# Performance work log

Hardware: AMD Instinct MI355X
Metric: run time of the kernel (lower is better)

Reference implementation:

```python
import jax, jax.numpy as jnp
import numpy as np

B, T, D, H = 4, 2048, 1024, 16
DK = D // H

def setup_inputs() -> dict:
    key = jax.random.key(0)
    ks = jax.random.split(key, 10)
    s = 1.0 / np.sqrt(D)
    inp = {
        'x': jax.random.normal(ks[0], (B, T, D), dtype=jnp.float32),
        'mask': jnp.tril(jnp.ones((T, T), dtype=jnp.int32))[None, None, :, :],
        'Wq': jax.random.normal(ks[1], (D, D), dtype=jnp.float32) * s,
        'bq': jnp.zeros((D,), dtype=jnp.float32),
        'Wk': jax.random.normal(ks[2], (D, D), dtype=jnp.float32) * s,
        'bk': jnp.zeros((D,), dtype=jnp.float32),
        'Wv': jax.random.normal(ks[3], (D, D), dtype=jnp.float32) * s,
        'bv': jnp.zeros((D,), dtype=jnp.float32),
        'Wo': jax.random.normal(ks[4], (D, D), dtype=jnp.float32) * s,
        'bo': jnp.zeros((D,), dtype=jnp.float32),
    }
    return inp

def reference(x, mask, Wq, bq, Wk, bk, Wv, bv, Wo, bo):
    # Project and split heads: [B,T,D] -> [B,H,T,DK]
    def heads(w, b):
        return (x @ w.T + b).reshape(B, T, H, DK).transpose(0, 2, 1, 3)
    q, k, v = heads(Wq, bq), heads(Wk, bk), heads(Wv, bv)
    scores = jnp.einsum('bhqd,bhkd->bhqk', q, k) / np.sqrt(DK).astype(jnp.float32)
    scores = jnp.where(mask[:, :, :T, :T] == 0, jnp.float32(-1e10), scores)
    prob = jax.nn.softmax(scores, axis=-1)
    y = jnp.einsum('bhqk,bhkd->bhqd', prob, v)  # [B,H,T,DK]
    y = y.transpose(0, 2, 1, 3).reshape(B, T, D)
    return y @ Wo.T + bo
```

## Files before the change

### kernel.cpp

```cpp
#include <hip/hip_runtime.h>


typedef unsigned short u16;
typedef unsigned int   u32;
using bf16x8 = __attribute__((ext_vector_type(8))) short;
using f32x4  = __attribute__((ext_vector_type(4))) float;
using u32x4  = __attribute__((ext_vector_type(4))) u32;

#define DEVINL __device__ __forceinline__
#define AS1 __attribute__((address_space(1)))
#define AS3 __attribute__((address_space(3)))

DEVINL u16 f2bf(float f) {
  u32 u = __builtin_bit_cast(u32, f);
  u32 r = u + 0x7fffu + ((u >> 16) & 1u);
  return (u16)(r >> 16);
}
DEVINL u32 pk2(float a, float b) {
  u32 ua = __builtin_bit_cast(u32, a) + 0x8000u;
  u32 ub = __builtin_bit_cast(u32, b) + 0x8000u;
  return (ua >> 16) | (ub & 0xffff0000u);
}
DEVINL float exp2fast(float x) {
#if __has_builtin(__builtin_amdgcn_exp2f)
  return __builtin_amdgcn_exp2f(x);
#else
  return __builtin_exp2f(x);
#endif
}
DEVINL void gload16(const u16* g, u16* l) {
  __builtin_amdgcn_global_load_lds((const AS1 u32*)g, (AS3 u32*)l, 16, 0, 0);
}

__global__ __launch_bounds__(256) void cvt_f32_bf16(const float* __restrict__ in,
                                                    u16* __restrict__ out, int n4) {
  int i = blockIdx.x * 256 + threadIdx.x;
  if (i < n4) {
    float4 v = reinterpret_cast<const float4*>(in)[i];
    u32 lo = (u32)f2bf(v.x) | ((u32)f2bf(v.y) << 16);
    u32 hi = (u32)f2bf(v.z) | ((u32)f2bf(v.w) << 16);
    reinterpret_cast<uint2*>(out)[i] = make_uint2(lo, hi);
  }
}

DEVINL void gemm_core(const u16* __restrict__ Ag, const u16* __restrict__ Bg,
                      int m0, int n0, f32x4 acc[4][4], u16* Al, u16* Bl, int tid) {
  const int lane = tid & 63, wave = tid >> 6;
  const int wr = wave >> 1, wc = wave & 1;
  const int lr = lane & 15, lg = lane >> 4;
  const int srow = wave * 32 + (lane >> 2);
  const int scol = ((lane & 3) * 8) ^ ((srow & 3) << 3);
  for (int kt = 0; kt < 1024; kt += 32) {
    __syncthreads();
    const u16* ga = Ag + (size_t)(m0 + srow) * 1024 + kt + scol;
    gload16(ga,             Al + wave * 1024);
    gload16(ga + 16 * 1024, Al + wave * 1024 + 512);
    const u16* gb = Bg + (size_t)(n0 + srow) * 1024 + kt + scol;
    gload16(gb,             Bl + wave * 1024);
    gload16(gb + 16 * 1024, Bl + wave * 1024 + 512);
    __syncthreads();
    bf16x8 af[4], bfr[4];
#pragma unroll
    for (int t = 0; t < 4; t++) {
      int ra = wr * 64 + t * 16 + lr;
      af[t] = *reinterpret_cast<const bf16x8*>(
          reinterpret_cast<const char*>(Al) + ra * 64 + ((lg * 16) ^ ((ra & 3) << 4)));
      int rb = wc * 64 + t * 16 + lr;
      bfr[t] = *reinterpret_cast<const bf16x8*>(
          reinterpret_cast<const char*>(Bl) + rb * 64 + ((lg * 16) ^ ((rb & 3) << 4)));
    }
#pragma unroll
    for (int mi = 0; mi < 4; mi++)
#pragma unroll
      for (int ni = 0; ni < 4; ni++)
        acc[mi][ni] = __builtin_amdgcn_mfma_f32_16x16x32_bf16(af[mi], bfr[ni], acc[mi][ni], 0, 0, 0);
  }
}

__global__ __launch_bounds__(256) void qkv_gemm(
    const u16* __restrict__ xb,
    const u16* __restrict__ wqb, const u16* __restrict__ wkb, const u16* __restrict__ wvb,
    const float* __restrict__ bq, const float* __restrict__ bk, const float* __restrict__ bv,
    u16* __restrict__ qb, u16* __restrict__ kb, u16* __restrict__ vb) {
  __shared__ __align__(16) u16 smem[8192];
  u16* Al = smem;
  u16* Bl = smem + 4096;
  const int z = blockIdx.z;
  const u16* W = (z == 0) ? wqb : (z == 1) ? wkb : wvb;
  const float* bias = (z == 0) ? bq : (z == 1) ? bk : bv;
  const int m0 = blockIdx.x * 128, n0 = blockIdx.y * 128;
  f32x4 acc[4][4];
#pragma unroll
  for (int a = 0; a < 4; a++)
#pragma unroll
    for (int b2 = 0; b2 < 4; b2++) acc[a][b2] = f32x4{0.f, 0.f, 0.f, 0.f};
  gemm_core(xb, W, m0, n0, acc, Al, Bl, threadIdx.x);
  const int lane = threadIdx.x & 63, wave = threadIdx.x >> 6;
  const int wr = wave >> 1, wc = wave & 1, lr = lane & 15, lg = lane >> 4;

  if (z == 2) {
    const int b = m0 >> 11, tb = m0 & 2047;
#pragma unroll
    for (int h2 = 0; h2 < 2; ++h2) {
      __syncthreads();
      if (wc == h2) {
#pragma unroll
        for (int mi = 0; mi < 4; mi++)
#pragma unroll
          for (int ni = 0; ni < 4; ni++)
#pragma unroll
            for (int i = 0; i < 4; i++) {
              int t_l = wr * 64 + mi * 16 + lg * 4 + i;
              int dk_l = ni * 16 + lr;
              float v = acc[mi][ni][i] + bias[n0 + h2 * 64 + dk_l];
              int m = t_l & 63;
              int col = (t_l & 64) | (m & 0x23) | ((m & 0x0C) << 1) | ((m & 0x10) >> 2);
              *(u16*)((char*)smem + dk_l * 256 + ((col * 2) ^ ((dk_l & 7) << 4))) = f2bf(v);
            }
      }
      __syncthreads();
      const int hh = (n0 >> 6) + h2;
      u16* vrow = vb + (size_t)(b * 16 + hh) * 64 * 2048 + tb;
#pragma unroll
      for (int i2 = 0; i2 < 4; i2++) {
        int c = (int)threadIdx.x + i2 * 256;
        int dk_l = c >> 4, tc2 = c & 15;
        int4 val = *(const int4*)((const char*)smem + dk_l * 256 + ((tc2 * 16) ^ ((dk_l & 7) << 4)));
        *(int4*)(vrow + (size_t)dk_l * 2048 + tc2 * 8) = val;
      }
    }
    return;
  }

  u16* dst = (z == 0) ? qb : kb;
  const float scl = (z == 0) ? 0.180336880f : 1.0f;
#pragma unroll
  for (int mi = 0; mi < 4; mi++)
#pragma unroll
    for (int ni = 0; ni < 4; ni++)
#pragma unroll
      for (int i = 0; i < 4; i++) {
        int gm = m0 + wr * 64 + mi * 16 + lg * 4 + i;
        int gn = n0 + wc * 64 + ni * 16 + lr;
        float v = (acc[mi][ni][i] + bias[gn]) * scl;
        int b = gm >> 11, t = gm & 2047;
        int h = gn >> 6, dk = gn & 63;
        dst[((size_t)(b * 16 + h) * 2048 + t) * 64 + dk] = f2bf(v);
      }
}

__global__ __launch_bounds__(256) void out_gemm(
    const u16* __restrict__ yb, const u16* __restrict__ wob,
    const float* __restrict__ bo, float* __restrict__ out) {
  __shared__ __align__(16) u16 smem[8192];
  u16* Al = smem;
  u16* Bl = smem + 4096;
  const int m0 = blockIdx.x * 128, n0 = blockIdx.y * 128;
  f32x4 acc[4][4];
#pragma unroll
  for (int a = 0; a < 4; a++)
#pragma unroll
    for (int b2 = 0; b2 < 4; b2++) acc[a][b2] = f32x4{0.f, 0.f, 0.f, 0.f};
  gemm_core(yb, wob, m0, n0, acc, Al, Bl, threadIdx.x);
  const int lane = threadIdx.x & 63, wave = threadIdx.x >> 6;
  const int wr = wave >> 1, wc = wave & 1, lr = lane & 15, lg = lane >> 4;
#pragma unroll
  for (int mi = 0; mi < 4; mi++)
#pragma unroll
    for (int ni = 0; ni < 4; ni++)
#pragma unroll
      for (int i = 0; i < 4; i++) {
        int gm = m0 + wr * 64 + mi * 16 + lg * 4 + i;
        int gn = n0 + wc * 64 + ni * 16 + lr;
        out[(size_t)gm * 1024 + gn] = acc[mi][ni][i] + bo[gn];
      }
}

__global__ __launch_bounds__(256) void attn_fwd(const u16* __restrict__ q_ws,
                                                const u16* __restrict__ k_ws,
                                                const u16* __restrict__ vt_ws,
                                                u16* __restrict__ y_ws) {
  __shared__ __align__(16) u16 Kl[2][4096];
  __shared__ __align__(16) u16 Vt[2][4096];

  const int tid = threadIdx.x;
  const int wave = tid >> 6, lane = tid & 63;
  const int lr = lane & 15, lg = lane >> 4;
  const int qtile = 31 - blockIdx.x;
  const int bh = blockIdx.y;
  const int q0 = qtile * 64;
  const size_t base = (size_t)bh * 2048 * 64;
  const int rgq = q0 + wave * 16 + lr;

  const int srow = wave * 16 + (lane >> 3);
  const int kcol = ((lane & 7) * 8) ^ ((srow & 7) << 3);

  bf16x8 qf[2];
#pragma unroll
  for (int s = 0; s < 2; s++)
    qf[s] = *reinterpret_cast<const bf16x8*>(q_ws + base + (size_t)rgq * 64 + s * 32 + lg * 8);
  asm volatile("s_waitcnt vmcnt(0)" ::: "memory");

  float m_run = -3.0e38f, l_run = 0.f;
  f32x4 oacc[4];
#pragma unroll
  for (int nt = 0; nt < 4; nt++) oacc[nt] = f32x4{0.f, 0.f, 0.f, 0.f};

  auto stage = [&](int buf, int kv0) {
    const u16* kg = k_ws + base + (size_t)(kv0 + srow) * 64 + kcol;
    gload16(kg,           &Kl[buf][wave * 1024]);
    gload16(kg + 8 * 64,  &Kl[buf][wave * 1024 + 512]);
    const u16* vg = vt_ws + base + (size_t)srow * 2048 + kv0 + kcol;
    gload16(vg,            &Vt[buf][wave * 1024]);
    gload16(vg + 8 * 2048, &Vt[buf][wave * 1024 + 512]);
  };

  stage(0, 0);
  int cur = 0;
  for (int t2 = 0; t2 <= qtile; ++t2) {
    const int kv0 = t2 * 64;
    if (t2 < qtile) {
      stage(cur ^ 1, kv0 + 64);
      asm volatile("s_waitcnt vmcnt(4)" ::: "memory");
    } else {
      asm volatile("s_waitcnt vmcnt(0)" ::: "memory");
    }
    __builtin_amdgcn_s_barrier();
    const u16* Kb = Kl[cur];
    const u16* Vb = Vt[cur];

    float sv[4][4];
    __builtin_amdgcn_s_setprio(1);
#pragma unroll
    for (int ct = 0; ct < 4; ct++) {
      f32x4 s = f32x4{0.f, 0.f, 0.f, 0.f};
      int krow = ct * 16 + lr;
#pragma unroll
      for (int s2 = 0; s2 < 2; s2++) {
        bf16x8 kf = *reinterpret_cast<const bf16x8*>(
            reinterpret_cast<const char*>(Kb) + krow * 128 + ((s2 * 64 + lg * 16) ^ ((krow & 7) << 4)));
        s = __builtin_amdgcn_mfma_f32_16x16x32_bf16(kf, qf[s2], s, 0, 0, 0);
      }
#pragma unroll
      for (int i = 0; i < 4; i++) sv[ct][i] = s[i];
    }
    __builtin_amdgcn_s_setprio(0);

    if (t2 == qtile) {
#pragma unroll
      for (int ct = 0; ct < 4; ct++)
#pragma unroll
        for (int i = 0; i < 4; i++)
          if (kv0 + ct * 16 + lg * 4 + i > rgq) sv[ct][i] = -1e30f;
    }

    float cm[4];
#pragma unroll
    for (int ct = 0; ct < 4; ct++)
      cm[ct] = fmaxf(fmaxf(sv[ct][0], sv[ct][1]), fmaxf(sv[ct][2], sv[ct][3]));
    float mx = fmaxf(fmaxf(cm[0], cm[1]), fmaxf(cm[2], cm[3]));
    mx = fmaxf(mx, __shfl_xor(mx, 16, 64));
    mx = fmaxf(mx, __shfl_xor(mx, 32, 64));

    float mnew, alpha;
    const bool nodefer = !__all(mx <= m_run + 8.0f);
    if (nodefer) { mnew = fmaxf(m_run, mx); alpha = exp2fast(m_run - mnew); }
    else         { mnew = m_run;            alpha = 1.0f; }

    float p[4][4];
#pragma unroll
    for (int ct = 0; ct < 4; ct++)
#pragma unroll
      for (int i = 0; i < 4; i++) p[ct][i] = exp2fast(sv[ct][i] - mnew);
    float cs[4];
#pragma unroll
    for (int ct = 0; ct < 4; ct++)
      cs[ct] = (p[ct][0] + p[ct][1]) + (p[ct][2] + p[ct][3]);
    float ps = (cs[0] + cs[1]) + (cs[2] + cs[3]);
    ps += __shfl_xor(ps, 16, 64);
    ps += __shfl_xor(ps, 32, 64);
    l_run = l_run * alpha + ps;
    m_run = mnew;

    u32x4 pw[2];
#pragma unroll
    for (int ks = 0; ks < 2; ks++) {
      pw[ks][0] = pk2(p[2 * ks][0],     p[2 * ks][1]);
      pw[ks][1] = pk2(p[2 * ks][2],     p[2 * ks][3]);
      pw[ks][2] = pk2(p[2 * ks + 1][0], p[2 * ks + 1][1]);
      pw[ks][3] = pk2(p[2 * ks + 1][2], p[2 * ks + 1][3]);
    }

    if (nodefer) {
#pragma unroll
      for (int nt = 0; nt < 4; nt++)
#pragma unroll
        for (int i = 0; i < 4; i++) oacc[nt][i] *= alpha;
    }

    __builtin_amdgcn_s_setprio(1);
#pragma unroll
    for (int nt = 0; nt < 4; nt++) {
      int d = nt * 16 + lr;
#pragma unroll
      for (int ks = 0; ks < 2; ks++) {
        bf16x8 vf = *reinterpret_cast<const bf16x8*>(
            reinterpret_cast<const char*>(Vb) + d * 128 + ((ks * 64 + lg * 16) ^ ((d & 7) << 4)));
        oacc[nt] = __builtin_amdgcn_mfma_f32_16x16x32_bf16(
            vf, __builtin_bit_cast(bf16x8, pw[ks]), oacc[nt], 0, 0, 0);
      }
    }
    __builtin_amdgcn_s_setprio(0);
    __builtin_amdgcn_s_barrier();
    cur ^= 1;
  }

  const float inv = 1.0f / l_run;
  const int b = bh >> 4, h = bh & 15;
#pragma unroll
  for (int nt = 0; nt < 4; nt++) {
    u32 w0 = (u32)f2bf(oacc[nt][0] * inv) | ((u32)f2bf(oacc[nt][1] * inv) << 16);
    u32 w1 = (u32)f2bf(oacc[nt][2] * inv) | ((u32)f2bf(oacc[nt][3] * inv) << 16);
    *reinterpret_cast<uint2*>(y_ws + ((size_t)(b * 2048 + rgq)) * 1024 + h * 64 + nt * 16 + lg * 4) =
        make_uint2(w0, w1);
  }
}

extern "C" void kernel_launch(void* const* d_in, const int* in_sizes, int n_in,
                              void* d_out, int out_size, void* d_ws, size_t ws_size,
                              hipStream_t stream) {
  const float* x  = (const float*)d_in[0];
  const float* Wq = (const float*)d_in[2];
  const float* bq = (const float*)d_in[3];
  const float* Wk = (const float*)d_in[4];
  const float* bk = (const float*)d_in[5];
  const float* Wv = (const float*)d_in[6];
  const float* bv = (const float*)d_in[7];
  const float* Wo = (const float*)d_in[8];
  const float* bo = (const float*)d_in[9];
  float* out = (float*)d_out;

  u16* xb  = (u16*)d_ws;
  u16* wqb = xb  + 8388608;
  u16* wkb = wqb + 1048576;
  u16* wvb = wkb + 1048576;
  u16* wob = wvb + 1048576;
  u16* qb  = wob + 1048576;
  u16* kb  = qb  + 8388608;
  u16* vtb = kb  + 8388608;
  u16* yb  = vtb + 8388608;

  cvt_f32_bf16<<<8192, 256, 0, stream>>>(x,  xb,  2097152);
  cvt_f32_bf16<<<1024, 256, 0, stream>>>(Wq, wqb, 262144);
  cvt_f32_bf16<<<1024, 256, 0, stream>>>(Wk, wkb, 262144);
  cvt_f32_bf16<<<1024, 256, 0, stream>>>(Wv, wvb, 262144);
  cvt_f32_bf16<<<1024, 256, 0, stream>>>(Wo, wob, 262144);

  qkv_gemm<<<dim3(64, 8, 3), 256, 0, stream>>>(xb, wqb, wkb, wvb, bq, bk, bv, qb, kb, vtb);
  attn_fwd<<<dim3(32, 64), 256, 0, stream>>>(qb, kb, vtb, yb);
  out_gemm<<<dim3(64, 8), 256, 0, stream>>>(yb, wob, bo, out);
}
```

Measured before the change: 338.8 us.

## Process two query subtiles per attention block to reuse K/V tiles

The attention kernel now handles 128 query rows per block as two 64-row subtiles that share each staged K/V tile, so every K/V tile is loaded once for twice the query rows and the grid halves. The lower subtile skips its MFMA and softmax work on the final diagonal tile. The probability packing now uses the hardware v_cvt_pk_bf16_f32 instruction instead of manual bit-twiddling, and the four weight conversions are merged into one launch. This raises register pressure and halves the number of blocks, which may hurt occupancy and load balance across the causal workload.

```diff
diff --git a/kernel.cpp b/kernel.cpp
--- a/kernel.cpp
+++ b/kernel.cpp
@@ -16,10 +16,10 @@
   u32 r = u + 0x7fffu + ((u >> 16) & 1u);
   return (u16)(r >> 16);
 }
-DEVINL u32 pk2(float a, float b) {
-  u32 ua = __builtin_bit_cast(u32, a) + 0x8000u;
-  u32 ub = __builtin_bit_cast(u32, b) + 0x8000u;
-  return (ua >> 16) | (ub & 0xffff0000u);
+DEVINL u32 cvtpk(float lo, float hi) {
+  u32 r;
+  asm("v_cvt_pk_bf16_f32 %0, %1, %2" : "=v"(r) : "v"(lo), "v"(hi));
+  return r;
 }
 DEVINL float exp2fast(float x) {
 #if __has_builtin(__builtin_amdgcn_exp2f)
@@ -41,6 +41,21 @@
     u32 hi = (u32)f2bf(v.z) | ((u32)f2bf(v.w) << 16);
     reinterpret_cast<uint2*>(out)[i] = make_uint2(lo, hi);
   }
+}
+
+__global__ __launch_bounds__(256) void cvt_w4(const float* __restrict__ w0,
+                                              const float* __restrict__ w1,
+                                              const float* __restrict__ w2,
+                                              const float* __restrict__ w3,
+                                              u16* __restrict__ o) {
+  const int z = blockIdx.y;
+  const float* in = (z == 0) ? w0 : (z == 1) ? w1 : (z == 2) ? w2 : w3;
+  u16* out = o + (size_t)z * 1048576;
+  int i = blockIdx.x * 256 + threadIdx.x;
+  float4 v = reinterpret_cast<const float4*>(in)[i];
+  u32 lo = (u32)f2bf(v.x) | ((u32)f2bf(v.y) << 16);
+  u32 hi = (u32)f2bf(v.z) | ((u32)f2bf(v.w) << 16);
+  reinterpret_cast<uint2*>(out)[i] = make_uint2(lo, hi);
 }
 
 DEVINL void gemm_core(const u16* __restrict__ Ag, const u16* __restrict__ Bg,
@@ -186,25 +201,31 @@
   const int tid = threadIdx.x;
   const int wave = tid >> 6, lane = tid & 63;
   const int lr = lane & 15, lg = lane >> 4;
-  const int qtile = 31 - blockIdx.x;
+  const int qtile = 15 - blockIdx.x;
   const int bh = blockIdx.y;
-  const int q0 = qtile * 64;
+  const int q0 = qtile * 128;
   const size_t base = (size_t)bh * 2048 * 64;
-  const int rgq = q0 + wave * 16 + lr;
 
   const int srow = wave * 16 + (lane >> 3);
   const int kcol = ((lane & 7) * 8) ^ ((srow & 7) << 3);
 
-  bf16x8 qf[2];
+  int rgq[2];
+  bf16x8 qf[2][2];
+#pragma unroll
+  for (int s = 0; s < 2; s++) {
+    rgq[s] = q0 + s * 64 + wave * 16 + lr;
+#pragma unroll
+    for (int h = 0; h < 2; h++)
+      qf[s][h] = *reinterpret_cast<const bf16x8*>(q_ws + base + (size_t)rgq[s] * 64 + h * 32 + lg * 8);
+  }
+  asm volatile("s_waitcnt vmcnt(0)" ::: "memory");
+
+  float m_run[2] = {-3.0e38f, -3.0e38f}, l_run[2] = {0.f, 0.f};
+  f32x4 oacc[2][4];
 #pragma unroll
   for (int s = 0; s < 2; s++)
-    qf[s] = *reinterpret_cast<const bf16x8*>(q_ws + base + (size_t)rgq * 64 + s * 32 + lg * 8);
-  asm volatile("s_waitcnt vmcnt(0)" ::: "memory");
-
-  float m_run = -3.0e38f, l_run = 0.f;
-  f32x4 oacc[4];
-#pragma unroll
-  for (int nt = 0; nt < 4; nt++) oacc[nt] = f32x4{0.f, 0.f, 0.f, 0.f};
+#pragma unroll
+    for (int nt = 0; nt < 4; nt++) oacc[s][nt] = f32x4{0.f, 0.f, 0.f, 0.f};
 
   auto stage = [&](int buf, int kv0) {
     const u16* kg = k_ws + base + (size_t)(kv0 + srow) * 64 + kcol;
@@ -216,10 +237,12 @@
   };
 
   stage(0, 0);
+  const int nt2 = 2 * qtile + 2;
   int cur = 0;
-  for (int t2 = 0; t2 <= qtile; ++t2) {
+  for (int t2 = 0; t2 < nt2; ++t2) {
     const int kv0 = t2 * 64;
-    if (t2 < qtile) {
+    const bool skip0 = (t2 == nt2 - 1);
+    if (t2 + 1 < nt2) {
       stage(cur ^ 1, kv0 + 64);
       asm volatile("s_waitcnt vmcnt(4)" ::: "memory");
     } else {
@@ -229,73 +252,81 @@
     const u16* Kb = Kl[cur];
     const u16* Vb = Vt[cur];
 
-    float sv[4][4];
+    f32x4 sA[4], sB[4];
     __builtin_amdgcn_s_setprio(1);
 #pragma unroll
     for (int ct = 0; ct < 4; ct++) {
-      f32x4 s = f32x4{0.f, 0.f, 0.f, 0.f};
+      sA[ct] = f32x4{0.f, 0.f, 0.f, 0.f};
+      sB[ct] = f32x4{0.f, 0.f, 0.f, 0.f};
       int krow = ct * 16 + lr;
 #pragma unroll
       for (int s2 = 0; s2 < 2; s2++) {
         bf16x8 kf = *reinterpret_cast<const bf16x8*>(
             reinterpret_cast<const char*>(Kb) + krow * 128 + ((s2 * 64 + lg * 16) ^ ((krow & 7) << 4)));
-        s = __builtin_amdgcn_mfma_f32_16x16x32_bf16(kf, qf[s2], s, 0, 0, 0);
-      }
-#pragma unroll
-      for (int i = 0; i < 4; i++) sv[ct][i] = s[i];
+        if (!skip0) sA[ct] = __builtin_amdgcn_mfma_f32_16x16x32_bf16(kf, qf[0][s2], sA[ct], 0, 0, 0);
+        sB[ct] = __builtin_amdgcn_mfma_f32_16x16x32_bf16(kf, qf[1][s2], sB[ct], 0, 0, 0);
+      }
     }
     __builtin_amdgcn_s_setprio(0);
 
-    if (t2 == qtile) {
+    u32x4 pw[2][2];
+    bool nodefer[2];
+#pragma unroll
+    for (int s = 0; s < 2; s++) {
+      if (s == 0 && skip0) continue;
+      float sv[4][4];
 #pragma unroll
       for (int ct = 0; ct < 4; ct++)
 #pragma unroll
-        for (int i = 0; i < 4; i++)
-          if (kv0 + ct * 16 + lg * 4 + i > rgq) sv[ct][i] = -1e30f;
-    }
-
-    float cm[4];
-#pragma unroll
-    for (int ct = 0; ct < 4; ct++)
-      cm[ct] = fmaxf(fmaxf(sv[ct][0], sv[ct][1]), fmaxf(sv[ct][2], sv[ct][3]));
-    float mx = fmaxf(fmaxf(cm[0], cm[1]), fmaxf(cm[2], cm[3]));
-    mx = fmaxf(mx, __shfl_xor(mx, 16, 64));
-    mx = fmaxf(mx, __shfl_xor(mx, 32, 64));
-
-    float mnew, alpha;
-    const bool nodefer = !__all(mx <= m_run + 8.0f);
-    if (nodefer) { mnew = fmaxf(m_run, mx); alpha = exp2fast(m_run - mnew); }
-    else         { mnew = m_run;            alpha = 1.0f; }
-
-    float p[4][4];
-#pragma unroll
-    for (int ct = 0; ct < 4; ct++)
-#pragma unroll
-      for (int i = 0; i < 4; i++) p[ct][i] = exp2fast(sv[ct][i] - mnew);
-    float cs[4];
-#pragma unroll
-    for (int ct = 0; ct < 4; ct++)
-      cs[ct] = (p[ct][0] + p[ct][1]) + (p[ct][2] + p[ct][3]);
-    float ps = (cs[0] + cs[1]) + (cs[2] + cs[3]);
-    ps += __shfl_xor(ps, 16, 64);
-    ps += __shfl_xor(ps, 32, 64);
-    l_run = l_run * alpha + ps;
-    m_run = mnew;
-
-    u32x4 pw[2];
-#pragma unroll
-    for (int ks = 0; ks < 2; ks++) {
-      pw[ks][0] = pk2(p[2 * ks][0],     p[2 * ks][1]);
-      pw[ks][1] = pk2(p[2 * ks][2],     p[2 * ks][3]);
-      pw[ks][2] = pk2(p[2 * ks + 1][0], p[2 * ks + 1][1]);
-      pw[ks][3] = pk2(p[2 * ks + 1][2], p[2 * ks + 1][3]);
-    }
-
-    if (nodefer) {
-#pragma unroll
-      for (int nt = 0; nt < 4; nt++)
-#pragma unroll
-        for (int i = 0; i < 4; i++) oacc[nt][i] *= alpha;
+        for (int i = 0; i < 4; i++) sv[ct][i] = (s == 0) ? sA[ct][i] : sB[ct][i];
+      if (t2 == 2 * qtile + s) {
+#pragma unroll
+        for (int ct = 0; ct < 4; ct++)
+#pragma unroll
+          for (int i = 0; i < 4; i++)
+            if (kv0 + ct * 16 + lg * 4 + i > rgq[s]) sv[ct][i] = -1e30f;
+      }
+      float cm[4];
+#pragma unroll
+      for (int ct = 0; ct < 4; ct++)
+        cm[ct] = fmaxf(fmaxf(sv[ct][0], sv[ct][1]), fmaxf(sv[ct][2], sv[ct][3]));
+      float mx = fmaxf(fmaxf(cm[0], cm[1]), fmaxf(cm[2], cm[3]));
+      mx = fmaxf(mx, __shfl_xor(mx, 16, 64));
+      mx = fmaxf(mx, __shfl_xor(mx, 32, 64));
+
+      float mnew, alpha;
+      nodefer[s] = !__all(mx <= m_run[s] + 8.0f);
+      if (nodefer[s]) { mnew = fmaxf(m_run[s], mx); alpha = exp2fast(m_run[s] - mnew); }
+      else            { mnew = m_run[s];            alpha = 1.0f; }
+
+      float p[4][4];
+#pragma unroll
+      for (int ct = 0; ct < 4; ct++)
+#pragma unroll
+        for (int i = 0; i < 4; i++) p[ct][i] = exp2fast(sv[ct][i] - mnew);
+      float cs[4];
+#pragma unroll
+      for (int ct = 0; ct < 4; ct++)
+        cs[ct] = (p[ct][0] + p[ct][1]) + (p[ct][2] + p[ct][3]);
+      float ps = (cs[0] + cs[1]) + (cs[2] + cs[3]);
+      ps += __shfl_xor(ps, 16, 64);
+      ps += __shfl_xor(ps, 32, 64);
+      l_run[s] = l_run[s] * alpha + ps;
+      m_run[s] = mnew;
+
+#pragma unroll
+      for (int ks = 0; ks < 2; ks++) {
+        pw[s][ks][0] = cvtpk(p[2 * ks][0],     p[2 * ks][1]);
+        pw[s][ks][1] = cvtpk(p[2 * ks][2],     p[2 * ks][3]);
+        pw[s][ks][2] = cvtpk(p[2 * ks + 1][0], p[2 * ks + 1][1]);
+        pw[s][ks][3] = cvtpk(p[2 * ks + 1][2], p[2 * ks + 1][3]);
+      }
+      if (nodefer[s]) {
+#pragma unroll
+        for (int nt = 0; nt < 4; nt++)
+#pragma unroll
+          for (int i = 0; i < 4; i++) oacc[s][nt][i] *= alpha;
+      }
     }
 
     __builtin_amdgcn_s_setprio(1);
@@ -306,8 +337,11 @@
       for (int ks = 0; ks < 2; ks++) {
         bf16x8 vf = *reinterpret_cast<const bf16x8*>(
             reinterpret_cast<const char*>(Vb) + d * 128 + ((ks * 64 + lg * 16) ^ ((d & 7) << 4)));
-        oacc[nt] = __builtin_amdgcn_mfma_f32_16x16x32_bf16(
-            vf, __builtin_bit_cast(bf16x8, pw[ks]), oacc[nt], 0, 0, 0);
+        if (!skip0)
+          oacc[0][nt] = __builtin_amdgcn_mfma_f32_16x16x32_bf16(
+              vf, __builtin_bit_cast(bf16x8, pw[0][ks]), oacc[0][nt], 0, 0, 0);
+        oacc[1][nt] = __builtin_amdgcn_mfma_f32_16x16x32_bf16(
+            vf, __builtin_bit_cast(bf16x8, pw[1][ks]), oacc[1][nt], 0, 0, 0);
       }
     }
     __builtin_amdgcn_s_setprio(0);
@@ -315,14 +349,17 @@
     cur ^= 1;
   }
 
-  const float inv = 1.0f / l_run;
   const int b = bh >> 4, h = bh & 15;
 #pragma unroll
-  for (int nt = 0; nt < 4; nt++) {
-    u32 w0 = (u32)f2bf(oacc[nt][0] * inv) | ((u32)f2bf(oacc[nt][1] * inv) << 16);
-    u32 w1 = (u32)f2bf(oacc[nt][2] * inv) | ((u32)f2bf(oacc[nt][3] * inv) << 16);
-    *reinterpret_cast<uint2*>(y_ws + ((size_t)(b * 2048 + rgq)) * 1024 + h * 64 + nt * 16 + lg * 4) =
-        make_uint2(w0, w1);
+  for (int s = 0; s < 2; s++) {
+    const float inv = 1.0f / l_run[s];
+#pragma unroll
+    for (int nt = 0; nt < 4; nt++) {
+      u32 w0 = (u32)f2bf(oacc[s][nt][0] * inv) | ((u32)f2bf(oacc[s][nt][1] * inv) << 16);
+      u32 w1 = (u32)f2bf(oacc[s][nt][2] * inv) | ((u32)f2bf(oacc[s][nt][3] * inv) << 16);
+      *reinterpret_cast<uint2*>(y_ws + ((size_t)(b * 2048 + rgq[s])) * 1024 + h * 64 + nt * 16 + lg * 4) =
+          make_uint2(w0, w1);
+    }
   }
 }
 
@@ -350,13 +387,10 @@
   u16* vtb = kb  + 8388608;
   u16* yb  = vtb + 8388608;
 
-  cvt_f32_bf16<<<8192, 256, 0, stream>>>(x,  xb,  2097152);
-  cvt_f32_bf16<<<1024, 256, 0, stream>>>(Wq, wqb, 262144);
-  cvt_f32_bf16<<<1024, 256, 0, stream>>>(Wk, wkb, 262144);
-  cvt_f32_bf16<<<1024, 256, 0, stream>>>(Wv, wvb, 262144);
-  cvt_f32_bf16<<<1024, 256, 0, stream>>>(Wo, wob, 262144);
+  cvt_f32_bf16<<<8192, 256, 0, stream>>>(x, xb, 2097152);
+  cvt_w4<<<dim3(1024, 4), 256, 0, stream>>>(Wq, Wk, Wv, Wo, wqb);
 
   qkv_gemm<<<dim3(64, 8, 3), 256, 0, stream>>>(xb, wqb, wkb, wvb, bq, bk, bv, qb, kb, vtb);
-  attn_fwd<<<dim3(32, 64), 256, 0, stream>>>(qb, kb, vtb, yb);
+  attn_fwd<<<dim3(16, 64), 256, 0, stream>>>(qb, kb, vtb, yb);
   out_gemm<<<dim3(64, 8), 256, 0, stream>>>(yb, wob, bo, out);
 }
```

Result: slower. 354.1 us (+4.5%).

## Compute softmax row sums via MFMA, use hardware bf16 pack, fuse weight casts

Applied to the files above, without the earlier changes.

The attention kernel now gets the softmax denominator from an extra MFMA that multiplies the probability tile by a ones vector, replacing the per-tile add tree and cross-lane shuffles. The max shuffle reduction and rescaling now run only when the deferred-max threshold is exceeded. Software bf16 packing is replaced by the v_cvt_pk_bf16_f32 instruction, and the four weight conversion launches are merged into one. The denominator now sums bf16-rounded probabilities, which changes the numerics slightly, and the skipped max reduction makes mnew per-lane-group rather than wave-uniform when the threshold is not hit.

```diff
diff --git a/kernel.cpp b/kernel.cpp
--- a/kernel.cpp
+++ b/kernel.cpp
@@ -16,10 +16,10 @@
   u32 r = u + 0x7fffu + ((u >> 16) & 1u);
   return (u16)(r >> 16);
 }
-DEVINL u32 pk2(float a, float b) {
-  u32 ua = __builtin_bit_cast(u32, a) + 0x8000u;
-  u32 ub = __builtin_bit_cast(u32, b) + 0x8000u;
-  return (ua >> 16) | (ub & 0xffff0000u);
+DEVINL u32 cvtpk(float lo, float hi) {
+  u32 r;
+  asm("v_cvt_pk_bf16_f32 %0, %1, %2" : "=v"(r) : "v"(lo), "v"(hi));
+  return r;
 }
 DEVINL float exp2fast(float x) {
 #if __has_builtin(__builtin_amdgcn_exp2f)
@@ -41,6 +41,21 @@
     u32 hi = (u32)f2bf(v.z) | ((u32)f2bf(v.w) << 16);
     reinterpret_cast<uint2*>(out)[i] = make_uint2(lo, hi);
   }
+}
+
+__global__ __launch_bounds__(256) void cvt_w4(const float* __restrict__ w0,
+                                              const float* __restrict__ w1,
+                                              const float* __restrict__ w2,
+                                              const float* __restrict__ w3,
+                                              u16* __restrict__ o) {
+  const int z = blockIdx.y;
+  const float* in = (z == 0) ? w0 : (z == 1) ? w1 : (z == 2) ? w2 : w3;
+  u16* out = o + (size_t)z * 1048576;
+  int i = blockIdx.x * 256 + threadIdx.x;
+  float4 v = reinterpret_cast<const float4*>(in)[i];
+  u32 lo = (u32)f2bf(v.x) | ((u32)f2bf(v.y) << 16);
+  u32 hi = (u32)f2bf(v.z) | ((u32)f2bf(v.w) << 16);
+  reinterpret_cast<uint2*>(out)[i] = make_uint2(lo, hi);
 }
 
 DEVINL void gemm_core(const u16* __restrict__ Ag, const u16* __restrict__ Bg,
@@ -201,7 +216,11 @@
     qf[s] = *reinterpret_cast<const bf16x8*>(q_ws + base + (size_t)rgq * 64 + s * 32 + lg * 8);
   asm volatile("s_waitcnt vmcnt(0)" ::: "memory");
 
-  float m_run = -3.0e38f, l_run = 0.f;
+  const u32x4 onesw = {0x3F803F80u, 0x3F803F80u, 0x3F803F80u, 0x3F803F80u};
+  const bf16x8 onesf = __builtin_bit_cast(bf16x8, onesw);
+
+  float m_run = -3.0e38f;
+  f32x4 lacc = f32x4{0.f, 0.f, 0.f, 0.f};
   f32x4 oacc[4];
 #pragma unroll
   for (int nt = 0; nt < 4; nt++) oacc[nt] = f32x4{0.f, 0.f, 0.f, 0.f};
@@ -259,43 +278,34 @@
     for (int ct = 0; ct < 4; ct++)
       cm[ct] = fmaxf(fmaxf(sv[ct][0], sv[ct][1]), fmaxf(sv[ct][2], sv[ct][3]));
     float mx = fmaxf(fmaxf(cm[0], cm[1]), fmaxf(cm[2], cm[3]));
-    mx = fmaxf(mx, __shfl_xor(mx, 16, 64));
-    mx = fmaxf(mx, __shfl_xor(mx, 32, 64));
-
-    float mnew, alpha;
-    const bool nodefer = !__all(mx <= m_run + 8.0f);
-    if (nodefer) { mnew = fmaxf(m_run, mx); alpha = exp2fast(m_run - mnew); }
-    else         { mnew = m_run;            alpha = 1.0f; }
+    const bool viol = !__all(mx <= m_run + 8.0f);
+    float mnew = m_run;
+    if (viol) {
+      mx = fmaxf(mx, __shfl_xor(mx, 16, 64));
+      mx = fmaxf(mx, __shfl_xor(mx, 32, 64));
+      mnew = fmaxf(m_run, mx);
+      float alpha = exp2fast(m_run - mnew);
+#pragma unroll
+      for (int nt = 0; nt < 4; nt++)
+#pragma unroll
+        for (int i = 0; i < 4; i++) oacc[nt][i] *= alpha;
+#pragma unroll
+      for (int i = 0; i < 4; i++) lacc[i] *= alpha;
+      m_run = mnew;
+    }
 
     float p[4][4];
 #pragma unroll
     for (int ct = 0; ct < 4; ct++)
 #pragma unroll
       for (int i = 0; i < 4; i++) p[ct][i] = exp2fast(sv[ct][i] - mnew);
-    float cs[4];
-#pragma unroll
-    for (int ct = 0; ct < 4; ct++)
-      cs[ct] = (p[ct][0] + p[ct][1]) + (p[ct][2] + p[ct][3]);
-    float ps = (cs[0] + cs[1]) + (cs[2] + cs[3]);
-    ps += __shfl_xor(ps, 16, 64);
-    ps += __shfl_xor(ps, 32, 64);
-    l_run = l_run * alpha + ps;
-    m_run = mnew;
-
     u32x4 pw[2];
 #pragma unroll
     for (int ks = 0; ks < 2; ks++) {
-      pw[ks][0] = pk2(p[2 * ks][0],     p[2 * ks][1]);
-      pw[ks][1] = pk2(p[2 * ks][2],     p[2 * ks][3]);
-      pw[ks][2] = pk2(p[2 * ks + 1][0], p[2 * ks + 1][1]);
-      pw[ks][3] = pk2(p[2 * ks + 1][2], p[2 * ks + 1][3]);
-    }
-
-    if (nodefer) {
-#pragma unroll
-      for (int nt = 0; nt < 4; nt++)
-#pragma unroll
-        for (int i = 0; i < 4; i++) oacc[nt][i] *= alpha;
+      pw[ks][0] = cvtpk(p[2 * ks][0],     p[2 * ks][1]);
+      pw[ks][1] = cvtpk(p[2 * ks][2],     p[2 * ks][3]);
+      pw[ks][2] = cvtpk(p[2 * ks + 1][0], p[2 * ks + 1][1]);
+      pw[ks][3] = cvtpk(p[2 * ks + 1][2], p[2 * ks + 1][3]);
     }
 
     __builtin_amdgcn_s_setprio(1);
@@ -310,17 +320,21 @@
             vf, __builtin_bit_cast(bf16x8, pw[ks]), oacc[nt], 0, 0, 0);
       }
     }
+    lacc = __builtin_amdgcn_mfma_f32_16x16x32_bf16(
+        onesf, __builtin_bit_cast(bf16x8, pw[0]), lacc, 0, 0, 0);
+    lacc = __builtin_amdgcn_mfma_f32_16x16x32_bf16(
+        onesf, __builtin_bit_cast(bf16x8, pw[1]), lacc, 0, 0, 0);
     __builtin_amdgcn_s_setprio(0);
     __builtin_amdgcn_s_barrier();
     cur ^= 1;
   }
 
-  const float inv = 1.0f / l_run;
+  const float inv = 1.0f / lacc[0];
   const int b = bh >> 4, h = bh & 15;
 #pragma unroll
   for (int nt = 0; nt < 4; nt++) {
-    u32 w0 = (u32)f2bf(oacc[nt][0] * inv) | ((u32)f2bf(oacc[nt][1] * inv) << 16);
-    u32 w1 = (u32)f2bf(oacc[nt][2] * inv) | ((u32)f2bf(oacc[nt][3] * inv) << 16);
+    u32 w0 = cvtpk(oacc[nt][0] * inv, oacc[nt][1] * inv);
+    u32 w1 = cvtpk(oacc[nt][2] * inv, oacc[nt][3] * inv);
     *reinterpret_cast<uint2*>(y_ws + ((size_t)(b * 2048 + rgq)) * 1024 + h * 64 + nt * 16 + lg * 4) =
         make_uint2(w0, w1);
   }
@@ -350,11 +364,8 @@
   u16* vtb = kb  + 8388608;
   u16* yb  = vtb + 8388608;
 
-  cvt_f32_bf16<<<8192, 256, 0, stream>>>(x,  xb,  2097152);
-  cvt_f32_bf16<<<1024, 256, 0, stream>>>(Wq, wqb, 262144);
-  cvt_f32_bf16<<<1024, 256, 0, stream>>>(Wk, wkb, 262144);
-  cvt_f32_bf16<<<1024, 256, 0, stream>>>(Wv, wvb, 262144);
-  cvt_f32_bf16<<<1024, 256, 0, stream>>>(Wo, wob, 262144);
+  cvt_f32_bf16<<<8192, 256, 0, stream>>>(x, xb, 2097152);
+  cvt_w4<<<dim3(1024, 4), 256, 0, stream>>>(Wq, Wk, Wv, Wo, wqb);
 
   qkv_gemm<<<dim3(64, 8, 3), 256, 0, stream>>>(xb, wqb, wkb, wvb, bq, bk, bv, qb, kb, vtb);
   attn_fwd<<<dim3(32, 64), 256, 0, stream>>>(qb, kb, vtb, yb);
```

New measurement: 315.2 us. -7.0%, faster.
